# Performance work log

Hardware: AMD Instinct MI355X
Metric: run time of the kernel (lower is better)

## Reference

```python
import jax, jax.numpy as jnp
import numpy as np

B = 1024
NOISE_DIM = 100
EMBED_DIM = 16
HIDDEN = 256
MAX_ORDER = 7
OUT_SIZE = (2 ** (MAX_ORDER + 1) + 1)  # 257
OUT_DIM = OUT_SIZE * OUT_SIZE           # 66049


def setup_inputs() -> dict:
    key = jax.random.key(0)
    ks = jax.random.split(key, 10)
    s = 0.02  # small init so sigmoid outputs are well-conditioned
    noise = jax.random.normal(ks[0], (B, NOISE_DIM), dtype=jnp.float32)
    # torch.stack in the original requires a homogeneous-order batch; use max order.
    orders = jnp.full((B,), MAX_ORDER, dtype=jnp.int32)
    embed_table = jax.random.normal(ks[1], (MAX_ORDER + 1, EMBED_DIM), dtype=jnp.float32)
    W1 = jax.random.normal(ks[2], (NOISE_DIM + EMBED_DIM, HIDDEN), dtype=jnp.float32) * s
    b1 = jnp.zeros((HIDDEN,), dtype=jnp.float32)
    W2 = jax.random.normal(ks[3], (HIDDEN, HIDDEN * 2), dtype=jnp.float32) * s
    b2 = jnp.zeros((HIDDEN * 2,), dtype=jnp.float32)
    W3 = jax.random.normal(ks[4], (HIDDEN * 2, HIDDEN * 4), dtype=jnp.float32) * s
    b3 = jnp.zeros((HIDDEN * 4,), dtype=jnp.float32)
    # expert head for the selected (homogeneous) order = MAX_ORDER
    W_out = jax.random.normal(ks[5], (HIDDEN * 4, OUT_DIM), dtype=jnp.float32) * s
    b_out = jnp.zeros((OUT_DIM,), dtype=jnp.float32)
    return {
        "noise": noise, "orders": orders, "embed_table": embed_table,
        "W1": W1, "b1": b1, "W2": W2, "b2": b2, "W3": W3, "b3": b3,
        "W_out": W_out, "b_out": b_out,
    }


def reference(noise, orders, embed_table, W1, b1, W2, b2, W3, b3, W_out, b_out):
    # embed(orders) -> (B, EMBED_DIM), concat with noise
    e = embed_table[orders]
    x = jnp.concatenate([noise, e], axis=1)            # (B, 116)
    h = jax.nn.relu(x @ W1 + b1)                       # (B, 256)
    h = jax.nn.relu(h @ W2 + b2)                       # (B, 512)
    h = jax.nn.relu(h @ W3 + b3)                       # (B, 1024)
    # per-order expert head; batch is homogeneous (all orders == MAX_ORDER),
    # the only configuration in which the original torch.stack succeeds.
    out = jax.nn.sigmoid(h @ W_out + b_out)            # (B, 66049)
    return out.reshape(noise.shape[0], OUT_SIZE, OUT_SIZE)
```

## Files before the change

kernel.cpp:

```cpp
#include <hip/hip_runtime.h>

typedef float f32x4 __attribute__((ext_vector_type(4)));
typedef float f32x2 __attribute__((ext_vector_type(2)));
typedef short s16x8 __attribute__((ext_vector_type(8)));

#define N_OUT 66049
#define K_DIM 1024
#define NPANEL 517

__device__ __forceinline__ ushort f2bf(float f) {
    union { float f; unsigned u; } x; x.f = f;
    unsigned r = x.u + 0x7fffu + ((x.u >> 16) & 1u);
    return (ushort)(r >> 16);
}

__device__ __forceinline__ unsigned cvt_pk_bf16(float lo, float hi) {
    unsigned r;
    asm("v_cvt_pk_bf16_f32 %0, %1, %2" : "=v"(r) : "v"(lo), "v"(hi));
    return r;
}

__device__ __forceinline__ void lds_load16(const void* g, void* l) {
    auto gp = reinterpret_cast<const __attribute__((address_space(1))) char*>(
        reinterpret_cast<uintptr_t>(g));
    auto lp = reinterpret_cast<__attribute__((address_space(3))) char*>(
        reinterpret_cast<uintptr_t>(l));
    __builtin_amdgcn_global_load_lds(gp, lp, 16, 0, 0);
}

__device__ __forceinline__ void chain_body(
    int bid, int tid, char* smem,
    const float* __restrict__ noise, const int* __restrict__ orders,
    const float* __restrict__ emb,
    const float* __restrict__ W1, const float* __restrict__ b1,
    const float* __restrict__ W2, const float* __restrict__ b2,
    const float* __restrict__ W3, const float* __restrict__ b3,
    ushort* __restrict__ h3)
{
    float* xs  = (float*)smem;
    float* h1s = (float*)(smem + 1920);
    float* h2s = (float*)(smem + 6016);
    const int R0 = bid * 4;

    for (int i = tid; i < 4 * 116; i += 256) {
        const int r = i / 116, c = i - r * 116;
        xs[r * 120 + c] = (c < 100) ? noise[(R0 + r) * 100 + c]
                                    : emb[orders[R0 + r] * 16 + (c - 100)];
    }
    __syncthreads();

    {
        const float bb = b1[tid];
        float a0 = bb, a1 = bb, a2 = bb, a3 = bb;
        #pragma unroll 4
        for (int k = 0; k < 116; ++k) {
            const float w = W1[k * 256 + tid];
            a0 = fmaf(xs[0 * 120 + k], w, a0);
            a1 = fmaf(xs[1 * 120 + k], w, a1);
            a2 = fmaf(xs[2 * 120 + k], w, a2);
            a3 = fmaf(xs[3 * 120 + k], w, a3);
        }
        h1s[0 * 256 + tid] = fmaxf(a0, 0.f);
        h1s[1 * 256 + tid] = fmaxf(a1, 0.f);
        h1s[2 * 256 + tid] = fmaxf(a2, 0.f);
        h1s[3 * 256 + tid] = fmaxf(a3, 0.f);
    }
    __syncthreads();

    {
        const f32x2 bb = *reinterpret_cast<const f32x2*>(&b2[tid * 2]);
        f32x2 a[4] = {bb, bb, bb, bb};
        for (int k = 0; k < 256; k += 4) {
            f32x4 hh[4];
            #pragma unroll
            for (int r = 0; r < 4; ++r) hh[r] = *reinterpret_cast<const f32x4*>(&h1s[r * 256 + k]);
            #pragma unroll
            for (int kk = 0; kk < 4; ++kk) {
                const f32x2 w = *reinterpret_cast<const f32x2*>(&W2[(k + kk) * 512 + tid * 2]);
                #pragma unroll
                for (int r = 0; r < 4; ++r) {
                    a[r][0] = fmaf(hh[r][kk], w[0], a[r][0]);
                    a[r][1] = fmaf(hh[r][kk], w[1], a[r][1]);
                }
            }
        }
        #pragma unroll
        for (int r = 0; r < 4; ++r) {
            h2s[r * 512 + tid * 2]     = fmaxf(a[r][0], 0.f);
            h2s[r * 512 + tid * 2 + 1] = fmaxf(a[r][1], 0.f);
        }
    }
    __syncthreads();

    {
        const f32x4 bb = *reinterpret_cast<const f32x4*>(&b3[tid * 4]);
        f32x4 a[4] = {bb, bb, bb, bb};
        for (int k = 0; k < 512; k += 4) {
            f32x4 hh[4];
            #pragma unroll
            for (int r = 0; r < 4; ++r) hh[r] = *reinterpret_cast<const f32x4*>(&h2s[r * 512 + k]);
            #pragma unroll
            for (int kk = 0; kk < 4; ++kk) {
                const f32x4 w = *reinterpret_cast<const f32x4*>(&W3[(k + kk) * 1024 + tid * 4]);
                #pragma unroll
                for (int r = 0; r < 4; ++r) {
                    a[r][0] = fmaf(hh[r][kk], w[0], a[r][0]);
                    a[r][1] = fmaf(hh[r][kk], w[1], a[r][1]);
                    a[r][2] = fmaf(hh[r][kk], w[2], a[r][2]);
                    a[r][3] = fmaf(hh[r][kk], w[3], a[r][3]);
                }
            }
        }
        #pragma unroll
        for (int r = 0; r < 4; ++r) {
            ushort4 u;
            u.x = f2bf(fmaxf(a[r][0], 0.f));
            u.y = f2bf(fmaxf(a[r][1], 0.f));
            u.z = f2bf(fmaxf(a[r][2], 0.f));
            u.w = f2bf(fmaxf(a[r][3], 0.f));
            *reinterpret_cast<ushort4*>(&h3[(size_t)(R0 + r) * 1024 + tid * 4]) = u;
        }
    }
}

__device__ __forceinline__ void convert_wout_body(
    int p, int kt, int tid, char* smem,
    const float* __restrict__ Wout, ushort* __restrict__ Bp)
{
    float* T = (float*)smem;
    const int k0 = kt * 64;

    if (p < NPANEL - 1) {
        const int c4 = (tid & 31) * 4;
        const int r0 = tid >> 5;
        const float* src = Wout + (size_t)k0 * N_OUT + (size_t)p * 128 + c4;
        #pragma unroll
        for (int i = 0; i < 8; ++i) {
            const int r = r0 + i * 8;
            f32x4 v = __builtin_nontemporal_load(
                reinterpret_cast<const f32x4*>(src + (size_t)r * N_OUT));
            *reinterpret_cast<f32x4*>(&T[r * 132 + c4]) = v;
        }
    } else {
        const int c = tid & 31, r0 = tid >> 5;
        #pragma unroll
        for (int i = 0; i < 8; ++i) {
            const int r = r0 + i * 8;
            #pragma unroll
            for (int j = 0; j < 4; ++j) {
                int col = p * 128 + c * 4 + j;
                if (col > N_OUT - 1) col = N_OUT - 1;
                T[r * 132 + c * 4 + j] = Wout[(size_t)(k0 + r) * N_OUT + col];
            }
        }
    }
    __syncthreads();

    const size_t base = ((size_t)p * 128 + kt * 8) * 128 * 8;
    #pragma unroll
    for (int i = 0; i < 4; ++i) {
        const int v = tid + i * 256;
        const int kbl = v >> 7, nl = v & 127;
        s16x8 o;
        #pragma unroll
        for (int j = 0; j < 8; ++j) o[j] = (short)f2bf(T[(kbl * 8 + j) * 132 + nl]);
        *reinterpret_cast<s16x8*>(Bp + base + (size_t)v * 8) = o;
    }
}

__global__ __launch_bounds__(256) void prep(
    const float* __restrict__ noise, const int* __restrict__ orders,
    const float* __restrict__ emb,
    const float* __restrict__ W1, const float* __restrict__ b1,
    const float* __restrict__ W2, const float* __restrict__ b2,
    const float* __restrict__ W3, const float* __restrict__ b3,
    const float* __restrict__ Wout,
    ushort* __restrict__ h3, ushort* __restrict__ Bp)
{
    __shared__ __align__(16) char smem[33792];
    const int bx = blockIdx.x;
    const int tid = threadIdx.x;
    if (bx < 256) {
        chain_body(bx, tid, smem, noise, orders, emb, W1, b1, W2, b2, W3, b3, h3);
    } else {
        const int c = bx - 256;
        const int p  = c % NPANEL;
        const int kt = c / NPANEL;
        convert_wout_body(p, kt, tid, smem, Wout, Bp);
    }
}

__global__ __launch_bounds__(256, 4) void gemm_out(
    const ushort* __restrict__ h3, const ushort* __restrict__ Bp,
    const float* __restrict__ bout, float* __restrict__ out)
{
    __shared__ __align__(16) char smem[33792];
    ushort* Alds = (ushort*)smem;
    ushort* Blds = (ushort*)(smem + 16384);

    const int tid = threadIdx.x;
    const int lane = tid & 63;
    const int w = tid >> 6;
    const int wm = w >> 1, wn = w & 1;

    const int raw = blockIdx.x;
    const int panel = (raw >> 6) * 8 + (raw & 7);
    const int mblk = (raw >> 3) & 7;
    if (panel >= NPANEL) return;
    const int m0 = mblk * 128;
    const int n0 = panel * 128;

    f32x4 acc[4][4] = {};

    const int arow = wm * 64 + (lane & 15);
    const int ac0  = lane >> 4;
    const int bn   = wn * 64 + (lane & 15);

    const ushort* BpPanel = Bp + (size_t)panel * (128 * 128 * 8);

    for (int kt = 0; kt < 16; ++kt) {
        const int k0 = kt * 64;
        #pragma unroll
        for (int i = 0; i < 4; ++i) {
            const int u = (w * 4 + i) * 64 + lane;
            const int r = u >> 3, cc = u & 7;
            const ushort* src = h3 + (size_t)(m0 + r) * K_DIM + (k0 + ((cc ^ (r & 7)) << 3));
            lds_load16(src, (void*)&Alds[(w * 4 + i) * 512]);
        }
        const ushort* bsrc = BpPanel + (size_t)kt * 8192;
        #pragma unroll
        for (int i = 0; i < 4; ++i) {
            const int u = (w * 4 + i) * 64 + lane;
            lds_load16(bsrc + (size_t)u * 8, (void*)&Blds[(w * 4 + i) * 512]);
        }
        __syncthreads();

        #pragma unroll
        for (int ks = 0; ks < 2; ++ks) {
            s16x8 af[4], bfr[4];
            #pragma unroll
            for (int fm = 0; fm < 4; ++fm) {
                const int r = arow + fm * 16;
                const int cc = (ks * 4 + ac0) ^ (r & 7);
                af[fm] = *reinterpret_cast<const s16x8*>(&Alds[r * 64 + cc * 8]);
            }
            const int kbl = ks * 4 + ac0;
            #pragma unroll
            for (int fn = 0; fn < 4; ++fn)
                bfr[fn] = *reinterpret_cast<const s16x8*>(&Blds[(kbl * 128 + bn + fn * 16) * 8]);
            #pragma unroll
            for (int fm = 0; fm < 4; ++fm)
                #pragma unroll
                for (int fn = 0; fn < 4; ++fn)
                    acc[fm][fn] = __builtin_amdgcn_mfma_f32_16x16x32_bf16(
                        af[fm], bfr[fn], acc[fm][fn], 0, 0, 0);
        }
        __syncthreads();
    }

    if (n0 + 128 <= N_OUT) {
        float bo[4];
        #pragma unroll
        for (int fn = 0; fn < 4; ++fn) bo[fn] = bout[n0 + wn * 64 + fn * 16 + (lane & 15)];
        float* Elds = (float*)smem;
        #pragma unroll
        for (int p = 0; p < 2; ++p) {
            if (wm == p) {
                #pragma unroll
                for (int fm = 0; fm < 4; ++fm)
                    #pragma unroll
                    for (int fn = 0; fn < 4; ++fn)
                        #pragma unroll
                        for (int j = 0; j < 4; ++j) {
                            const int rl = fm * 16 + (lane >> 4) * 4 + j;
                            const int cl = wn * 64 + fn * 16 + (lane & 15);
                            const float z = acc[fm][fn][j] + bo[fn];
                            Elds[rl * 132 + cl] = 1.f / (1.f + __expf(-z));
                        }
            }
            __syncthreads();
            const size_t gb = (size_t)(m0 + p * 64) * N_OUT + n0;
            const int g = tid >> 5, c4 = (tid & 31) * 4;
            #pragma unroll
            for (int i = 0; i < 8; ++i) {
                const int rl = i * 8 + g;
                const f32x4 v = *reinterpret_cast<const f32x4*>(&Elds[rl * 132 + c4]);
                __builtin_nontemporal_store(v,
                    reinterpret_cast<f32x4*>(&out[gb + (size_t)rl * N_OUT + c4]));
            }
            __syncthreads();
        }
    } else {
        const int rbase = m0 + wm * 64 + (lane >> 4) * 4;
        #pragma unroll
        for (int fn = 0; fn < 4; ++fn) {
            const int col = n0 + wn * 64 + fn * 16 + (lane & 15);
            const bool ok = col < N_OUT;
            const float bo = bout[ok ? col : (N_OUT - 1)];
            #pragma unroll
            for (int fm = 0; fm < 4; ++fm) {
                #pragma unroll
                for (int j = 0; j < 4; ++j) {
                    if (ok) {
                        const int row = rbase + fm * 16 + j;
                        const float z = acc[fm][fn][j] + bo;
                        out[(size_t)row * N_OUT + col] = 1.f / (1.f + __expf(-z));
                    }
                }
            }
        }
    }
}

__global__ __launch_bounds__(256) void gemm_out_fused(
    const ushort* __restrict__ h3, const float* __restrict__ Wout,
    const float* __restrict__ bout, float* __restrict__ out)
{
    __shared__ __align__(16) char smem[33792];
    ushort* Alds = (ushort*)smem;
    ushort* Blds = (ushort*)(smem + 16384);

    const int tid = threadIdx.x;
    const int lane = tid & 63;
    const int w = tid >> 6;
    const int wm = w >> 1, wn = w & 1;

    const int raw = blockIdx.x;
    const int panel = (raw >> 6) * 8 + (raw & 7);
    const int mblk = (raw >> 3) & 7;
    if (panel >= NPANEL) return;
    const int m0 = mblk * 128;
    const int n0 = panel * 128;

    const int nl = tid & 127;
    const int kb0 = tid >> 7;
    int nc = n0 + nl; if (nc > N_OUT - 1) nc = N_OUT - 1;
    const float* Bsrc = Wout + nc;

    f32x4 acc[4][4] = {};
    float breg[32];

    const int arow = wm * 64 + (lane & 15);
    const int ac0  = lane >> 4;
    const int bn   = wn * 64 + (lane & 15);

    auto stageA = [&](int kt) {
        const int k0 = kt * 64;
        #pragma unroll
        for (int i = 0; i < 4; ++i) {
            const int u = (w * 4 + i) * 64 + lane;
            const int r = u >> 3, cc = u & 7;
            const ushort* src = h3 + (size_t)(m0 + r) * K_DIM + (k0 + ((cc ^ (r & 7)) << 3));
            lds_load16(src, (void*)&Alds[(w * 4 + i) * 512]);
        }
    };
    auto loadB = [&](int kt) {
        const int k0 = kt * 64;
        #pragma unroll
        for (int g = 0; g < 4; ++g) {
            const int kb = kb0 + g * 2;
            #pragma unroll
            for (int i = 0; i < 8; ++i)
                breg[g * 8 + i] = Bsrc[(size_t)(k0 + kb * 8 + i) * N_OUT];
        }
    };
    auto writeB = [&]() {
        #pragma unroll
        for (int g = 0; g < 4; ++g) {
            const int kb = kb0 + g * 2;
            union { s16x8 v; unsigned u[4]; } pk;
            #pragma unroll
            for (int h = 0; h < 4; ++h)
                pk.u[h] = cvt_pk_bf16(breg[g * 8 + 2 * h], breg[g * 8 + 2 * h + 1]);
            *reinterpret_cast<s16x8*>(&Blds[(kb * 128 + nl) * 8]) = pk.v;
        }
    };
    auto compute = [&]() {
        #pragma unroll
        for (int ks = 0; ks < 2; ++ks) {
            s16x8 af[4], bfr[4];
            #pragma unroll
            for (int fm = 0; fm < 4; ++fm) {
                const int r = arow + fm * 16;
                const int cc = (ks * 4 + ac0) ^ (r & 7);
                af[fm] = *reinterpret_cast<const s16x8*>(&Alds[r * 64 + cc * 8]);
            }
            const int kb = ks * 4 + ac0;
            #pragma unroll
            for (int fn = 0; fn < 4; ++fn)
                bfr[fn] = *reinterpret_cast<const s16x8*>(&Blds[(kb * 128 + bn + fn * 16) * 8]);
            #pragma unroll
            for (int fm = 0; fm < 4; ++fm)
                #pragma unroll
                for (int fn = 0; fn < 4; ++fn)
                    acc[fm][fn] = __builtin_amdgcn_mfma_f32_16x16x32_bf16(
                        af[fm], bfr[fn], acc[fm][fn], 0, 0, 0);
        }
    };

    stageA(0);
    loadB(0);
    asm volatile("s_waitcnt vmcnt(0)" ::: "memory");
    asm volatile("s_barrier" ::: "memory");
    writeB();
    loadB(1);
    asm volatile("s_waitcnt lgkmcnt(0)" ::: "memory");
    asm volatile("s_barrier" ::: "memory");

    for (int kt = 0; kt < 16; ++kt) {
        compute();
        asm volatile("s_barrier" ::: "memory");
        if (kt < 15) {
            stageA(kt + 1);
            __builtin_amdgcn_sched_barrier(0);
            writeB();
            if (kt < 14) {
                loadB(kt + 2);
                asm volatile("s_waitcnt lgkmcnt(0)" ::: "memory");
                asm volatile("s_waitcnt vmcnt(32)" ::: "memory");
            } else {
                asm volatile("s_waitcnt lgkmcnt(0)" ::: "memory");
                asm volatile("s_waitcnt vmcnt(0)" ::: "memory");
            }
            asm volatile("s_barrier" ::: "memory");
        }
    }

    if (n0 + 128 <= N_OUT) {
        float bo[4];
        #pragma unroll
        for (int fn = 0; fn < 4; ++fn) bo[fn] = bout[n0 + wn * 64 + fn * 16 + (lane & 15)];
        float* Elds = (float*)smem;
        #pragma unroll
        for (int p = 0; p < 2; ++p) {
            if (wm == p) {
                #pragma unroll
                for (int fm = 0; fm < 4; ++fm)
                    #pragma unroll
                    for (int fn = 0; fn < 4; ++fn)
                        #pragma unroll
                        for (int j = 0; j < 4; ++j) {
                            const int rl = fm * 16 + (lane >> 4) * 4 + j;
                            const int cl = wn * 64 + fn * 16 + (lane & 15);
                            const float z = acc[fm][fn][j] + bo[fn];
                            Elds[rl * 132 + cl] = 1.f / (1.f + __expf(-z));
                        }
            }
            __syncthreads();
            const size_t gb = (size_t)(m0 + p * 64) * N_OUT + n0;
            const int g = tid >> 5, c4 = (tid & 31) * 4;
            #pragma unroll
            for (int i = 0; i < 8; ++i) {
                const int rl = i * 8 + g;
                const f32x4 v = *reinterpret_cast<const f32x4*>(&Elds[rl * 132 + c4]);
                *reinterpret_cast<f32x4*>(&out[gb + (size_t)rl * N_OUT + c4]) = v;
            }
            __syncthreads();
        }
    } else {
        const int rbase = m0 + wm * 64 + (lane >> 4) * 4;
        #pragma unroll
        for (int fn = 0; fn < 4; ++fn) {
            const int col = n0 + wn * 64 + fn * 16 + (lane & 15);
            const bool ok = col < N_OUT;
            const float bo = bout[ok ? col : (N_OUT - 1)];
            #pragma unroll
            for (int fm = 0; fm < 4; ++fm) {
                #pragma unroll
                for (int j = 0; j < 4; ++j) {
                    if (ok) {
                        const int row = rbase + fm * 16 + j;
                        const float z = acc[fm][fn][j] + bo;
                        out[(size_t)row * N_OUT + col] = 1.f / (1.f + __expf(-z));
                    }
                }
            }
        }
    }
}

extern "C" void kernel_launch(void* const* d_in, const int* in_sizes, int n_in,
                              void* d_out, int out_size, void* d_ws, size_t ws_size,
                              hipStream_t stream)
{
    const float* noise = (const float*)d_in[0];
    const int*   orders = (const int*)d_in[1];
    const float* emb   = (const float*)d_in[2];
    const float* W1 = (const float*)d_in[3];
    const float* b1 = (const float*)d_in[4];
    const float* W2 = (const float*)d_in[5];
    const float* b2 = (const float*)d_in[6];
    const float* W3 = (const float*)d_in[7];
    const float* b3 = (const float*)d_in[8];
    const float* Wout = (const float*)d_in[9];
    const float* bout = (const float*)d_in[10];

    char* ws = (char*)d_ws;
    ushort* h3 = (ushort*)ws;
    ushort* Bp = (ushort*)(ws + 0x200000);
    const size_t need = 0x200000 + (size_t)NPANEL * 128 * 128 * 8 * 2;
    const bool pre = (ws_size >= need);

    if (pre) {
        prep<<<256 + NPANEL * 16, 256, 0, stream>>>(
            noise, orders, emb, W1, b1, W2, b2, W3, b3, Wout, h3, Bp);
        gemm_out<<<4160, 256, 0, stream>>>(h3, Bp, bout, (float*)d_out);
    } else {
        prep<<<256, 256, 0, stream>>>(
            noise, orders, emb, W1, b1, W2, b2, W3, b3, Wout, h3, Bp);
        gemm_out_fused<<<4160, 256, 0, stream>>>(h3, Wout, bout, (float*)d_out);
    }
}
```

Measured before the change: 305.3 us.

## Load B fragments directly to registers and pipeline A staging across k-tiles

The output GEMM no longer stages the pre-packed W_out panel through LDS. Each thread loads its B fragments straight from global memory into registers, so only A goes through LDS. The loop is restructured with manual waitcnt/s_barrier and sched_barriers so the next tile's A and B loads are issued right after compute, aiming to overlap loads with synchronization and cut LDS traffic. This raises register pressure, so launch bounds drop to 3 waves per EU, and the hand-written waitcnt counts must match the actual number of outstanding loads.

```diff
diff --git a/kernel.cpp b/kernel.cpp
--- a/kernel.cpp
+++ b/kernel.cpp
@@ -190,18 +190,18 @@
     }
 }
 
-__global__ __launch_bounds__(256, 4) void gemm_out(
+__global__ __launch_bounds__(256, 3) void gemm_out(
     const ushort* __restrict__ h3, const ushort* __restrict__ Bp,
     const float* __restrict__ bout, float* __restrict__ out)
 {
     __shared__ __align__(16) char smem[33792];
     ushort* Alds = (ushort*)smem;
-    ushort* Blds = (ushort*)(smem + 16384);
 
     const int tid = threadIdx.x;
     const int lane = tid & 63;
     const int w = tid >> 6;
     const int wm = w >> 1, wn = w & 1;
+    const int u4 = lane >> 4, l15 = lane & 15;
 
     const int raw = blockIdx.x;
     const int panel = (raw >> 6) * 8 + (raw & 7);
@@ -211,57 +211,76 @@
     const int n0 = panel * 128;
 
     f32x4 acc[4][4] = {};
-
-    const int arow = wm * 64 + (lane & 15);
-    const int ac0  = lane >> 4;
-    const int bn   = wn * 64 + (lane & 15);
+    s16x8 bfr[4][2];
+
+    const int arow = wm * 64 + l15;
+    const int bn   = wn * 64 + l15;
 
     const ushort* BpPanel = Bp + (size_t)panel * (128 * 128 * 8);
-
-    for (int kt = 0; kt < 16; ++kt) {
+    const ushort* Bth = BpPanel + ((size_t)(u4 << 7) + bn) * 8;
+
+    auto stageA = [&](int kt) {
         const int k0 = kt * 64;
         #pragma unroll
         for (int i = 0; i < 4; ++i) {
             const int u = (w * 4 + i) * 64 + lane;
             const int r = u >> 3, cc = u & 7;
-            const ushort* src = h3 + (size_t)(m0 + r) * K_DIM + (k0 + ((cc ^ (r & 7)) << 3));
+            const ushort* src = h3 + (((size_t)(m0 + r)) << 10) + (k0 + ((cc ^ (r & 7)) << 3));
             lds_load16(src, (void*)&Alds[(w * 4 + i) * 512]);
         }
-        const ushort* bsrc = BpPanel + (size_t)kt * 8192;
-        #pragma unroll
-        for (int i = 0; i < 4; ++i) {
-            const int u = (w * 4 + i) * 64 + lane;
-            lds_load16(bsrc + (size_t)u * 8, (void*)&Blds[(w * 4 + i) * 512]);
-        }
-        __syncthreads();
-
+    };
+    auto loadB = [&](int kt) {
+        const ushort* t0 = Bth + (size_t)kt * 8192;
+        #pragma unroll
+        for (int ks = 0; ks < 2; ++ks)
+            #pragma unroll
+            for (int fn = 0; fn < 4; ++fn)
+                bfr[fn][ks] = *reinterpret_cast<const s16x8*>(t0 + ks * 4096 + fn * 128);
+    };
+    auto compute = [&]() {
         #pragma unroll
         for (int ks = 0; ks < 2; ++ks) {
-            s16x8 af[4], bfr[4];
+            s16x8 af[4];
             #pragma unroll
             for (int fm = 0; fm < 4; ++fm) {
                 const int r = arow + fm * 16;
-                const int cc = (ks * 4 + ac0) ^ (r & 7);
+                const int cc = (ks * 4 + u4) ^ (r & 7);
                 af[fm] = *reinterpret_cast<const s16x8*>(&Alds[r * 64 + cc * 8]);
             }
-            const int kbl = ks * 4 + ac0;
-            #pragma unroll
-            for (int fn = 0; fn < 4; ++fn)
-                bfr[fn] = *reinterpret_cast<const s16x8*>(&Blds[(kbl * 128 + bn + fn * 16) * 8]);
             #pragma unroll
             for (int fm = 0; fm < 4; ++fm)
                 #pragma unroll
                 for (int fn = 0; fn < 4; ++fn)
                     acc[fm][fn] = __builtin_amdgcn_mfma_f32_16x16x32_bf16(
-                        af[fm], bfr[fn], acc[fm][fn], 0, 0, 0);
-        }
-        __syncthreads();
+                        af[fm], bfr[fn][ks], acc[fm][fn], 0, 0, 0);
+        }
+    };
+
+    stageA(0);
+    __builtin_amdgcn_sched_barrier(0);
+    loadB(0);
+    __builtin_amdgcn_sched_barrier(0);
+    asm volatile("s_waitcnt vmcnt(8)" ::: "memory");
+    asm volatile("s_barrier" ::: "memory");
+
+    for (int kt = 0; kt < 16; ++kt) {
+        compute();
+        asm volatile("s_waitcnt lgkmcnt(0)" ::: "memory");
+        asm volatile("s_barrier" ::: "memory");
+        if (kt < 15) {
+            stageA(kt + 1);
+            __builtin_amdgcn_sched_barrier(0);
+            loadB(kt + 1);
+            __builtin_amdgcn_sched_barrier(0);
+            asm volatile("s_waitcnt vmcnt(8)" ::: "memory");
+            asm volatile("s_barrier" ::: "memory");
+        }
     }
 
     if (n0 + 128 <= N_OUT) {
         float bo[4];
         #pragma unroll
-        for (int fn = 0; fn < 4; ++fn) bo[fn] = bout[n0 + wn * 64 + fn * 16 + (lane & 15)];
+        for (int fn = 0; fn < 4; ++fn) bo[fn] = bout[n0 + wn * 64 + fn * 16 + l15];
         float* Elds = (float*)smem;
         #pragma unroll
         for (int p = 0; p < 2; ++p) {
@@ -272,8 +291,8 @@
                     for (int fn = 0; fn < 4; ++fn)
                         #pragma unroll
                         for (int j = 0; j < 4; ++j) {
-                            const int rl = fm * 16 + (lane >> 4) * 4 + j;
-                            const int cl = wn * 64 + fn * 16 + (lane & 15);
+                            const int rl = fm * 16 + u4 * 4 + j;
+                            const int cl = wn * 64 + fn * 16 + l15;
                             const float z = acc[fm][fn][j] + bo[fn];
                             Elds[rl * 132 + cl] = 1.f / (1.f + __expf(-z));
                         }
@@ -291,10 +310,10 @@
             __syncthreads();
         }
     } else {
-        const int rbase = m0 + wm * 64 + (lane >> 4) * 4;
+        const int rbase = m0 + wm * 64 + u4 * 4;
         #pragma unroll
         for (int fn = 0; fn < 4; ++fn) {
-            const int col = n0 + wn * 64 + fn * 16 + (lane & 15);
+            const int col = n0 + wn * 64 + fn * 16 + l15;
             const bool ok = col < N_OUT;
             const float bo = bout[ok ? col : (N_OUT - 1)];
             #pragma unroll
```

Measured after the change: 310.9 us. No clear change (+1.8%).
